# Performance work log

Measured on AMD Instinct MI355X. Metric: run time of the kernel, lower is better.

The kernel has to match this reference:

```python
import jax, jax.numpy as jnp
import numpy as np

V, E, H, OUT, L = 32000, 512, 512, 2, 2
S, B = 512, 64


def setup_inputs() -> dict:
    key = jax.random.key(0)
    ks = jax.random.split(key, 8)
    sc_w = float(np.sqrt(6.0 / (H + (E + H))))  # xavier_uniform bound-ish scale
    inp = {
        "texts": jax.random.randint(ks[0], (S, B), 0, V, dtype=jnp.int64),
        "emb": jax.random.normal(ks[1], (V, E), jnp.float32) * 0.05,
        "Wf": jax.random.normal(ks[2], (L, H, E + H), jnp.float32) * sc_w,
        "bf": jnp.zeros((L, H, 1), jnp.float32),
        "Wi": jax.random.normal(ks[3], (L, H, E + H), jnp.float32) * sc_w,
        "bi": jnp.zeros((L, H, 1), jnp.float32),
        "Wo": jax.random.normal(ks[4], (L, H, E + H), jnp.float32) * sc_w,
        "bo": jnp.zeros((L, H, 1), jnp.float32),
        "Wc": jax.random.normal(ks[5], (L, H, E + H), jnp.float32) * sc_w,
        "bc": jnp.zeros((L, H, 1), jnp.float32),
        "Wy": jax.random.normal(ks[6], (OUT, H), jnp.float32) * 0.05,
        "by": jnp.zeros((OUT, 1), jnp.float32),
    }
    return inp


def reference(texts, emb, Wf, bf, Wi, bi, Wo, bo, Wc, bc, Wy, by):
    seq_len, batch = texts.shape
    num_layers, hidden = Wf.shape[0], Wf.shape[1]
    # embedded: [S, E, B] (matches torch permute(1,2,0) of [B,S,E])
    x_seq = jnp.transpose(emb[texts], (0, 2, 1))

    h0 = jnp.zeros((hidden, batch), x_seq.dtype)
    c0 = jnp.zeros((hidden, batch), x_seq.dtype)

    def step(carry, x):
        h, c = carry  # NOTE: single (h, c) shared across layers, as in source
        for l in range(num_layers):
            cat = jnp.concatenate([h, x], axis=0)  # [H+E, B]
            ft = jax.nn.sigmoid(Wf[l] @ cat + bf[l])
            it = jax.nn.sigmoid(Wi[l] @ cat + bi[l])
            chat = jnp.tanh(Wc[l] @ cat + bc[l])
            c = ft * c + it * chat
            ot = jax.nn.sigmoid(Wo[l] @ cat + bo[l])
            h = ot * jnp.tanh(c)
            x = h
        return (h, c), None

    (h, _), _ = jax.lax.scan(step, (h0, c0), x_seq)
    y = h.T @ Wy.T + by.T  # [B, OUT]
    return jnp.squeeze(y, axis=1) if y.shape[1] == 1 else y
```

## Files before the change

kernel.cpp:

```cpp
#include <hip/hip_runtime.h>


typedef _Float16 f16;
typedef _Float16 f16x8 __attribute__((ext_vector_type(8)));
typedef float f32x4 __attribute__((ext_vector_type(4)));
typedef unsigned int u32;
typedef unsigned long long u64;
typedef unsigned short u16;

constexpr int Hn = 512, En = 512, Bn = 64, Sn = 512, OUTn = 2;
constexpr int NG = 4, GB = 32, BS = 16, RPB = 16;
constexpr int NB = NG * GB;
constexpr int NT = 512;
constexpr int RING = 16;
constexpr u32 SENT = 0xFFFFFFFFu;

constexpr size_t XB_OFF = 0;
constexpr size_t XB_SZ  = (size_t)NG * Sn * 16 * 64 * 16;
constexpr size_t RG_OFF = XB_OFF + XB_SZ;
constexpr size_t RG_SZ  = (size_t)NG * RING * 16384;

__device__ __forceinline__ float sig_(float x) { return 1.f / (1.f + expf(-x)); }

__device__ __forceinline__ void astore(u32* p, u32 v) {
  __hip_atomic_store(p, v, __ATOMIC_RELAXED, __HIP_MEMORY_SCOPE_AGENT);
}
__device__ __forceinline__ u64 aload64(const u64* p) {
  return __hip_atomic_load(p, __ATOMIC_RELAXED, __HIP_MEMORY_SCOPE_AGENT);
}
__device__ __forceinline__ bool okw(u64 x) {
  return ((u32)x != SENT) && ((u32)(x >> 32) != SENT);
}

__device__ __forceinline__ void poll2x(const u32* p0, const u32* p1, f16x8& a, f16x8& b) {
  union { f16x8 v; u32 d[4]; } ua, ub;
  int guard = 0;
  do {
    asm volatile("global_load_dwordx4 %0, %2, off sc1\n\t"
                 "global_load_dwordx4 %1, %3, off sc1\n\t"
                 "s_waitcnt vmcnt(0)"
                 : "=&v"(ua.v), "=&v"(ub.v) : "v"(p0), "v"(p1) : "memory");
    if ((ua.d[0] != SENT) & (ua.d[1] != SENT) & (ua.d[2] != SENT) & (ua.d[3] != SENT) &
        (ub.d[0] != SENT) & (ub.d[1] != SENT) & (ub.d[2] != SENT) & (ub.d[3] != SENT)) break;
  } while (++guard < (1 << 17));
  a = ua.v; b = ub.v;
}

union uf16 { f16 f; u16 u; };

__device__ __forceinline__ int fl_idx(int k, int col) {
  return (((k >> 5) * 64 + (((k >> 3) & 3) * 16) + col) << 3) + (k & 7);
}

__global__ void __launch_bounds__(256) xb_fill(
    const int* __restrict__ texts, const float* __restrict__ emb,
    f16x8* __restrict__ xb)
{
  const int bidx = blockIdx.x;
  const int g = bidx >> 9, t = bidx & (Sn - 1);
  const int tid = threadIdx.x;
  f16x8* dst = xb + (size_t)bidx * 1024;
  for (int slot = tid; slot < 1024; slot += 256) {
    int s = slot >> 6, sl = slot & 63, kg = sl >> 4, b = sl & 15;
    int idx = texts[t * Bn + g * BS + b];
    const float* er = emb + (size_t)idx * En + s * 32 + kg * 8;
    f16x8 v;
    #pragma unroll
    for (int j = 0; j < 8; ++j) v[j] = (f16)er[j];
    dst[slot] = v;
  }
}

__global__ void __launch_bounds__(NT) lstm_mfma(
    const float* __restrict__ Wf, const float* __restrict__ bf,
    const float* __restrict__ Wi, const float* __restrict__ bi,
    const float* __restrict__ Wo, const float* __restrict__ bo,
    const float* __restrict__ Wc, const float* __restrict__ bc,
    const float* __restrict__ Wy, const float* __restrict__ by,
    float* __restrict__ out, const f16x8* __restrict__ xb,
    u32* __restrict__ ringBase)
{
  __shared__ f16x8 sWAh[4][16][64];
  __shared__ float sAccP[8][64][17];
  __shared__ float sAccX[64][17];
  __shared__ float sBiasX[64], sBias1[64];
  __shared__ float sC[16][16];
  __shared__ float sRed[16][2][4];

  const int tid = threadIdx.x;
  const int bid = blockIdx.x;
  const int g = bid & 3;
  const int rank = bid >> 2;
  const int w = tid >> 6, l = tid & 63;
  const int col = l & 15, rb = (l >> 4) << 2;

  const float* Wg[4] = {Wf, Wi, Wc, Wo};
  const float* Bg[4] = {bf, bi, bc, bo};

  u32* ringG = ringBase + (size_t)g * RING * 4096;
  const f16x8* xbG = xb + (size_t)g * Sn * 1024;

  for (int i = 0; i < 8; ++i) {
    int slot = tid * 8 + i;
    int sl = slot & 63, ss = (slot >> 6) & 15, m4 = slot >> 10;
    const float* row = Wg[m4] + (size_t)(rank * RPB + (sl & 15)) * (En + Hn);
    int k0 = ss * 32 + (sl >> 4) * 8;
    f16x8 v;
    #pragma unroll
    for (int j = 0; j < 8; ++j) v[j] = (f16)row[k0 + j];
    sWAh[m4][ss][sl] = v;
  }
  f16x8 afr1[4][2];
  #pragma unroll
  for (int m = 0; m < 4; ++m) {
    const float* row = Wg[m] + (size_t)(Hn + rank * RPB + (l & 15)) * (En + Hn);
    #pragma unroll
    for (int i = 0; i < 2; ++i) {
      int k0 = (2 * w + i) * 32 + (l >> 4) * 8;
      f16x8 v;
      #pragma unroll
      for (int j = 0; j < 8; ++j) v[j] = (f16)(row[k0 + j] + row[k0 + j + Hn]);
      afr1[m][i] = v;
    }
  }
  f16x8 axf[16];
  if (w >= 4) {
    const float* row = Wg[w - 4] + (size_t)(rank * RPB + (l & 15)) * (En + Hn);
    #pragma unroll
    for (int i = 0; i < 16; ++i) {
      int k0 = Hn + i * 32 + (l >> 4) * 8;
      f16x8 v;
      #pragma unroll
      for (int j = 0; j < 8; ++j) v[j] = (f16)row[k0 + j];
      axf[i] = v;
    }
  }
  if (tid < 64) {
    int gate = tid >> 4, hr = tid & 15;
    sBiasX[tid] = Bg[gate][rank * RPB + hr];
    sBias1[tid] = Bg[gate][Hn + rank * RPB + hr];
  }
  if (tid < 256) sC[tid >> 4][tid & 15] = 0.f;
  __syncthreads();

  if (w >= 4) {
    f32x4 ax = {0.f, 0.f, 0.f, 0.f};
    #pragma unroll
    for (int s = 0; s < 16; ++s)
      ax = __builtin_amdgcn_mfma_f32_16x16x32_f16(axf[s], xbG[s * 64 + l], ax, 0, 0, 0);
    #pragma unroll
    for (int v = 0; v < 4; ++v) sAccX[(w - 4) * 16 + rb + v][col] = ax[v];
  }

  for (int t = 0; t < Sn; ++t) {
    u32* rdA = ringG + (size_t)((2 * t) & 15) * 4096;
    u32* wrA = ringG + (size_t)((2 * t + 1) & 15) * 4096;
    u32* clA = ringG + (size_t)((2 * t + 9) & 15) * 4096;

    {
      f16x8 b0, b1;
      poll2x(rdA + (2 * w * 64 + l) * 4, rdA + ((2 * w + 1) * 64 + l) * 4, b0, b1);
      if (tid >= 128 && tid < 256) astore(clA + rank * 128 + (tid - 128), SENT);
      f32x4 a0 = {0.f, 0.f, 0.f, 0.f}, a1 = a0, a2 = a0, a3 = a0;
      a0 = __builtin_amdgcn_mfma_f32_16x16x32_f16(sWAh[0][2 * w][l], b0, a0, 0, 0, 0);
      a1 = __builtin_amdgcn_mfma_f32_16x16x32_f16(sWAh[1][2 * w][l], b0, a1, 0, 0, 0);
      a2 = __builtin_amdgcn_mfma_f32_16x16x32_f16(sWAh[2][2 * w][l], b0, a2, 0, 0, 0);
      a3 = __builtin_amdgcn_mfma_f32_16x16x32_f16(sWAh[3][2 * w][l], b0, a3, 0, 0, 0);
      a0 = __builtin_amdgcn_mfma_f32_16x16x32_f16(sWAh[0][2 * w + 1][l], b1, a0, 0, 0, 0);
      a1 = __builtin_amdgcn_mfma_f32_16x16x32_f16(sWAh[1][2 * w + 1][l], b1, a1, 0, 0, 0);
      a2 = __builtin_amdgcn_mfma_f32_16x16x32_f16(sWAh[2][2 * w + 1][l], b1, a2, 0, 0, 0);
      a3 = __builtin_amdgcn_mfma_f32_16x16x32_f16(sWAh[3][2 * w + 1][l], b1, a3, 0, 0, 0);
      #pragma unroll
      for (int v = 0; v < 4; ++v) {
        sAccP[w][ 0 + rb + v][col] = a0[v];
        sAccP[w][16 + rb + v][col] = a1[v];
        sAccP[w][32 + rb + v][col] = a2[v];
        sAccP[w][48 + rb + v][col] = a3[v];
      }
    }
    __syncthreads();
    if (tid < 128) {
      int q8 = tid >> 4, b = tid & 15;
      u32 pk = 0;
      #pragma unroll
      for (int j = 0; j < 2; ++j) {
        int hr = 2 * q8 + j;
        float af = sAccX[ 0 + hr][b] + sBiasX[ 0 + hr];
        float ai = sAccX[16 + hr][b] + sBiasX[16 + hr];
        float ac = sAccX[32 + hr][b] + sBiasX[32 + hr];
        float ao = sAccX[48 + hr][b] + sBiasX[48 + hr];
        #pragma unroll
        for (int ww = 0; ww < 8; ++ww) {
          af += sAccP[ww][ 0 + hr][b];
          ai += sAccP[ww][16 + hr][b];
          ac += sAccP[ww][32 + hr][b];
          ao += sAccP[ww][48 + hr][b];
        }
        float ft = sig_(af), it = sig_(ai), ch = tanhf(ac), ot = sig_(ao);
        float c = ft * sC[hr][b] + it * ch;
        sC[hr][b] = c;
        uf16 hv; hv.f = (f16)(ot * tanhf(c));
        pk |= (u32)hv.u << (16 * j);
      }
      int k0 = rank * RPB + 2 * q8;
      int slot = (k0 >> 5) * 64 + ((k0 >> 3) & 3) * 16 + b;
      astore(wrA + slot * 4 + (q8 & 3), pk);
    }

    u32* wrB = ringG + (size_t)((2 * t + 2) & 15) * 4096;
    u32* clB = ringG + (size_t)((2 * t + 10) & 15) * 4096;
    {
      f16x8 b0, b1;
      poll2x(wrA + (2 * w * 64 + l) * 4, wrA + ((2 * w + 1) * 64 + l) * 4, b0, b1);
      if (tid >= 128 && tid < 256) astore(clB + rank * 128 + (tid - 128), SENT);
      f32x4 a0 = {0.f, 0.f, 0.f, 0.f}, a1 = a0, a2 = a0, a3 = a0;
      a0 = __builtin_amdgcn_mfma_f32_16x16x32_f16(afr1[0][0], b0, a0, 0, 0, 0);
      a1 = __builtin_amdgcn_mfma_f32_16x16x32_f16(afr1[1][0], b0, a1, 0, 0, 0);
      a2 = __builtin_amdgcn_mfma_f32_16x16x32_f16(afr1[2][0], b0, a2, 0, 0, 0);
      a3 = __builtin_amdgcn_mfma_f32_16x16x32_f16(afr1[3][0], b0, a3, 0, 0, 0);
      a0 = __builtin_amdgcn_mfma_f32_16x16x32_f16(afr1[0][1], b1, a0, 0, 0, 0);
      a1 = __builtin_amdgcn_mfma_f32_16x16x32_f16(afr1[1][1], b1, a1, 0, 0, 0);
      a2 = __builtin_amdgcn_mfma_f32_16x16x32_f16(afr1[2][1], b1, a2, 0, 0, 0);
      a3 = __builtin_amdgcn_mfma_f32_16x16x32_f16(afr1[3][1], b1, a3, 0, 0, 0);
      #pragma unroll
      for (int v = 0; v < 4; ++v) {
        sAccP[w][ 0 + rb + v][col] = a0[v];
        sAccP[w][16 + rb + v][col] = a1[v];
        sAccP[w][32 + rb + v][col] = a2[v];
        sAccP[w][48 + rb + v][col] = a3[v];
      }
    }
    __syncthreads();
    if (tid < 128) {
      int q8 = tid >> 4, b = tid & 15;
      u32 pk = 0;
      #pragma unroll
      for (int j = 0; j < 2; ++j) {
        int hr = 2 * q8 + j;
        float af = sBias1[ 0 + hr];
        float ai = sBias1[16 + hr];
        float ac = sBias1[32 + hr];
        float ao = sBias1[48 + hr];
        #pragma unroll
        for (int ww = 0; ww < 8; ++ww) {
          af += sAccP[ww][ 0 + hr][b];
          ai += sAccP[ww][16 + hr][b];
          ac += sAccP[ww][32 + hr][b];
          ao += sAccP[ww][48 + hr][b];
        }
        float ft = sig_(af), it = sig_(ai), ch = tanhf(ac), ot = sig_(ao);
        float c = ft * sC[hr][b] + it * ch;
        sC[hr][b] = c;
        uf16 hv; hv.f = (f16)(ot * tanhf(c));
        pk |= (u32)hv.u << (16 * j);
      }
      int k0 = rank * RPB + 2 * q8;
      int slot = (k0 >> 5) * 64 + ((k0 >> 3) & 3) * 16 + b;
      astore(wrB + slot * 4 + (q8 & 3), pk);
    }
    if (w >= 4 && t + 1 < Sn) {
      const f16x8* xbt = xbG + (size_t)(t + 1) * 1024;
      f32x4 ax = {0.f, 0.f, 0.f, 0.f};
      #pragma unroll
      for (int s = 0; s < 16; ++s)
        ax = __builtin_amdgcn_mfma_f32_16x16x32_f16(axf[s], xbt[s * 64 + l], ax, 0, 0, 0);
      #pragma unroll
      for (int v = 0; v < 4; ++v) sAccX[(w - 4) * 16 + rb + v][col] = ax[v];
    }
  }

  __syncthreads();
  if (rank == 0) {
    const u64* fin = (const u64*)ringG;
    u64* dst = (u64*)&sWAh[0][0][0];
    for (int i = tid; i < 2048; i += NT) {
      u64 v = aload64(fin + i);
      int guard = 0;
      while (!okw(v)) { v = aload64(fin + i); if (++guard > (1 << 17)) break; }
      dst[i] = v;
    }
  }
  __syncthreads();
  if (rank == 0 && tid < 128) {
    const f16* tmp = (const f16*)&sWAh[0][0][0];
    int b = tid >> 3, o = (tid >> 2) & 1, kc = tid & 3;
    float p = 0.f;
    for (int kk = 0; kk < 128; ++kk) {
      int k = kc * 128 + kk;
      p += (float)tmp[fl_idx(k, b)] * Wy[o * Hn + k];
    }
    sRed[b][o][kc] = p;
  }
  __syncthreads();
  if (rank == 0 && tid < 32) {
    int b2 = tid >> 1, o2 = tid & 1;
    float s = by[o2];
    #pragma unroll
    for (int q = 0; q < 4; ++q) s += sRed[b2][o2][q];
    out[(g * BS + b2) * OUTn + o2] = s;
  }
}

extern "C" void kernel_launch(void* const* d_in, const int* in_sizes, int n_in,
                              void* d_out, int out_size, void* d_ws, size_t ws_size,
                              hipStream_t stream) {
  const int*   texts = (const int*)d_in[0];
  const float* emb   = (const float*)d_in[1];
  const float* Wf    = (const float*)d_in[2];
  const float* bf    = (const float*)d_in[3];
  const float* Wi    = (const float*)d_in[4];
  const float* bi    = (const float*)d_in[5];
  const float* Wo    = (const float*)d_in[6];
  const float* bo    = (const float*)d_in[7];
  const float* Wc    = (const float*)d_in[8];
  const float* bc    = (const float*)d_in[9];
  const float* Wy    = (const float*)d_in[10];
  const float* by    = (const float*)d_in[11];
  float* out = (float*)d_out;

  f16x8* xbuf     = (f16x8*)((char*)d_ws + XB_OFF);
  u32*   ringBase = (u32*)((char*)d_ws + RG_OFF);

  hipMemsetAsync((void*)ringBase, 0xFF, RG_SZ, stream);
  for (int g = 0; g < NG; ++g)
    hipMemsetAsync((void*)((char*)ringBase + (size_t)g * RING * 16384), 0x00, 16384, stream);

  xb_fill<<<dim3(NG * Sn), dim3(256), 0, stream>>>(texts, emb, xbuf);

  void* args[] = {(void*)&Wf, (void*)&bf, (void*)&Wi, (void*)&bi,
                  (void*)&Wo, (void*)&bo, (void*)&Wc, (void*)&bc, (void*)&Wy, (void*)&by,
                  (void*)&out, (void*)&xbuf, (void*)&ringBase};
  hipLaunchCooperativeKernel((const void*)lstm_mfma, dim3(NB), dim3(NT), args, 0, stream);
}
```

Baseline: 2.597 ms.

## Use fast exp2/rcp activations, per-element 16-bit ring stores, and early sentinel clears

```diff
diff --git a/kernel.cpp b/kernel.cpp
--- a/kernel.cpp
+++ b/kernel.cpp
@@ -20,7 +20,13 @@
 constexpr size_t RG_OFF = XB_OFF + XB_SZ;
 constexpr size_t RG_SZ  = (size_t)NG * RING * 16384;
 
-__device__ __forceinline__ float sig_(float x) { return 1.f / (1.f + expf(-x)); }
+__device__ __forceinline__ float fsig(float x) {
+  return __builtin_amdgcn_rcpf(1.f + __builtin_amdgcn_exp2f(-1.4426950408889634f * x));
+}
+__device__ __forceinline__ float ftanh(float x) {
+  float e = __builtin_amdgcn_exp2f(2.8853900817779268f * x);
+  return 1.f - 2.f * __builtin_amdgcn_rcpf(e + 1.f);
+}
 
 __device__ __forceinline__ void astore(u32* p, u32 v) {
   __hip_atomic_store(p, v, __ATOMIC_RELAXED, __HIP_MEMORY_SCOPE_AGENT);
@@ -28,8 +34,15 @@
 __device__ __forceinline__ u64 aload64(const u64* p) {
   return __hip_atomic_load(p, __ATOMIC_RELAXED, __HIP_MEMORY_SCOPE_AGENT);
 }
+__device__ __forceinline__ bool okd(u32 d) {
+  return ((d & 0xFFFFu) != 0xFFFFu) & ((d >> 16) != 0xFFFFu);
+}
 __device__ __forceinline__ bool okw(u64 x) {
-  return ((u32)x != SENT) && ((u32)(x >> 32) != SENT);
+  return okd((u32)x) & okd((u32)(x >> 32));
+}
+__device__ __forceinline__ void st16(u16* p, u16 v) {
+  u32 vv = v;
+  asm volatile("global_store_short %0, %1, off sc1" :: "v"(p), "v"(vv) : "memory");
 }
 
 __device__ __forceinline__ void poll2x(const u32* p0, const u32* p1, f16x8& a, f16x8& b) {
@@ -40,8 +53,8 @@
                  "global_load_dwordx4 %1, %3, off sc1\n\t"
                  "s_waitcnt vmcnt(0)"
                  : "=&v"(ua.v), "=&v"(ub.v) : "v"(p0), "v"(p1) : "memory");
-    if ((ua.d[0] != SENT) & (ua.d[1] != SENT) & (ua.d[2] != SENT) & (ua.d[3] != SENT) &
-        (ub.d[0] != SENT) & (ub.d[1] != SENT) & (ub.d[2] != SENT) & (ub.d[3] != SENT)) break;
+    if (okd(ua.d[0]) & okd(ua.d[1]) & okd(ua.d[2]) & okd(ua.d[3]) &
+        okd(ub.d[0]) & okd(ub.d[1]) & okd(ub.d[2]) & okd(ub.d[3])) break;
   } while (++guard < (1 << 17));
   a = ua.v; b = ub.v;
 }
@@ -157,10 +170,10 @@
     u32* wrA = ringG + (size_t)((2 * t + 1) & 15) * 4096;
     u32* clA = ringG + (size_t)((2 * t + 9) & 15) * 4096;
 
+    if (tid >= 384) astore(clA + rank * 128 + (tid - 384), SENT);
     {
       f16x8 b0, b1;
       poll2x(rdA + (2 * w * 64 + l) * 4, rdA + ((2 * w + 1) * 64 + l) * 4, b0, b1);
-      if (tid >= 128 && tid < 256) astore(clA + rank * 128 + (tid - 128), SENT);
       f32x4 a0 = {0.f, 0.f, 0.f, 0.f}, a1 = a0, a2 = a0, a3 = a0;
       a0 = __builtin_amdgcn_mfma_f32_16x16x32_f16(sWAh[0][2 * w][l], b0, a0, 0, 0, 0);
       a1 = __builtin_amdgcn_mfma_f32_16x16x32_f16(sWAh[1][2 * w][l], b0, a1, 0, 0, 0);
@@ -179,40 +192,32 @@
       }
     }
     __syncthreads();
-    if (tid < 128) {
-      int q8 = tid >> 4, b = tid & 15;
-      u32 pk = 0;
-      #pragma unroll
-      for (int j = 0; j < 2; ++j) {
-        int hr = 2 * q8 + j;
-        float af = sAccX[ 0 + hr][b] + sBiasX[ 0 + hr];
-        float ai = sAccX[16 + hr][b] + sBiasX[16 + hr];
-        float ac = sAccX[32 + hr][b] + sBiasX[32 + hr];
-        float ao = sAccX[48 + hr][b] + sBiasX[48 + hr];
-        #pragma unroll
-        for (int ww = 0; ww < 8; ++ww) {
-          af += sAccP[ww][ 0 + hr][b];
-          ai += sAccP[ww][16 + hr][b];
-          ac += sAccP[ww][32 + hr][b];
-          ao += sAccP[ww][48 + hr][b];
-        }
-        float ft = sig_(af), it = sig_(ai), ch = tanhf(ac), ot = sig_(ao);
-        float c = ft * sC[hr][b] + it * ch;
-        sC[hr][b] = c;
-        uf16 hv; hv.f = (f16)(ot * tanhf(c));
-        pk |= (u32)hv.u << (16 * j);
+    if (tid < 256) {
+      int hr = tid >> 4, b = tid & 15;
+      float af = sAccX[ 0 + hr][b] + sBiasX[ 0 + hr];
+      float ai = sAccX[16 + hr][b] + sBiasX[16 + hr];
+      float ac = sAccX[32 + hr][b] + sBiasX[32 + hr];
+      float ao = sAccX[48 + hr][b] + sBiasX[48 + hr];
+      #pragma unroll
+      for (int ww = 0; ww < 8; ++ww) {
+        af += sAccP[ww][ 0 + hr][b];
+        ai += sAccP[ww][16 + hr][b];
+        ac += sAccP[ww][32 + hr][b];
+        ao += sAccP[ww][48 + hr][b];
       }
-      int k0 = rank * RPB + 2 * q8;
-      int slot = (k0 >> 5) * 64 + ((k0 >> 3) & 3) * 16 + b;
-      astore(wrA + slot * 4 + (q8 & 3), pk);
+      float ft = fsig(af), it = fsig(ai), ch = ftanh(ac), ot = fsig(ao);
+      float c = ft * sC[hr][b] + it * ch;
+      sC[hr][b] = c;
+      uf16 hv; hv.f = (f16)(ot * ftanh(c));
+      st16((u16*)wrA + fl_idx(rank * RPB + hr, b), hv.u);
     }
 
     u32* wrB = ringG + (size_t)((2 * t + 2) & 15) * 4096;
     u32* clB = ringG + (size_t)((2 * t + 10) & 15) * 4096;
+    if (tid >= 384) astore(clB + rank * 128 + (tid - 384), SENT);
     {
       f16x8 b0, b1;
       poll2x(wrA + (2 * w * 64 + l) * 4, wrA + ((2 * w + 1) * 64 + l) * 4, b0, b1);
-      if (tid >= 128 && tid < 256) astore(clB + rank * 128 + (tid - 128), SENT);
       f32x4 a0 = {0.f, 0.f, 0.f, 0.f}, a1 = a0, a2 = a0, a3 = a0;
       a0 = __builtin_amdgcn_mfma_f32_16x16x32_f16(afr1[0][0], b0, a0, 0, 0, 0);
       a1 = __builtin_amdgcn_mfma_f32_16x16x32_f16(afr1[1][0], b0, a1, 0, 0, 0);
@@ -231,32 +236,24 @@
       }
     }
     __syncthreads();
-    if (tid < 128) {
-      int q8 = tid >> 4, b = tid & 15;
-      u32 pk = 0;
-      #pragma unroll
-      for (int j = 0; j < 2; ++j) {
-        int hr = 2 * q8 + j;
-        float af = sBias1[ 0 + hr];
-        float ai = sBias1[16 + hr];
-        float ac = sBias1[32 + hr];
-        float ao = sBias1[48 + hr];
-        #pragma unroll
-        for (int ww = 0; ww < 8; ++ww) {
-          af += sAccP[ww][ 0 + hr][b];
-          ai += sAccP[ww][16 + hr][b];
-          ac += sAccP[ww][32 + hr][b];
-          ao += sAccP[ww][48 + hr][b];
-        }
-        float ft = sig_(af), it = sig_(ai), ch = tanhf(ac), ot = sig_(ao);
-        float c = ft * sC[hr][b] + it * ch;
-        sC[hr][b] = c;
-        uf16 hv; hv.f = (f16)(ot * tanhf(c));
-        pk |= (u32)hv.u << (16 * j);
+    if (tid < 256) {
+      int hr = tid >> 4, b = tid & 15;
+      float af = sBias1[ 0 + hr];
+      float ai = sBias1[16 + hr];
+      float ac = sBias1[32 + hr];
+      float ao = sBias1[48 + hr];
+      #pragma unroll
+      for (int ww = 0; ww < 8; ++ww) {
+        af += sAccP[ww][ 0 + hr][b];
+        ai += sAccP[ww][16 + hr][b];
+        ac += sAccP[ww][32 + hr][b];
+        ao += sAccP[ww][48 + hr][b];
       }
-      int k0 = rank * RPB + 2 * q8;
-      int slot = (k0 >> 5) * 64 + ((k0 >> 3) & 3) * 16 + b;
-      astore(wrB + slot * 4 + (q8 & 3), pk);
+      float ft = fsig(af), it = fsig(ai), ch = ftanh(ac), ot = fsig(ao);
+      float c = ft * sC[hr][b] + it * ch;
+      sC[hr][b] = c;
+      uf16 hv; hv.f = (f16)(ot * ftanh(c));
+      st16((u16*)wrB + fl_idx(rank * RPB + hr, b), hv.u);
     }
     if (w >= 4 && t + 1 < Sn) {
       const f16x8* xbt = xbG + (size_t)(t + 1) * 1024;
```

After: 2.564 ms. About the same (-1.3%).
